# Performance work log

Measured on AMD Instinct MI355X. Metric: run time of the kernel, lower is better.

The kernel has to match this reference:

```python
import jax, jax.numpy as jnp
import numpy as np

SPIKING_T = 8        # args['spiking_t']
V_TH = 1.0           # spikingjelly IFNode default v_threshold
TAU = 2.0            # NonSpikingLIFNode tau
ALPHA = 4.0          # spikingjelly default Sigmoid surrogate alpha
MIN_LOG_STD, MAX_LOG_STD = -20.0, 2.0
LOG_2PI = float(np.log(2.0 * np.pi))

@jax.custom_vjp
def spike(x):
    # Heaviside forward (spikingjelly surrogate.Sigmoid behavior)
    return (x >= 0.0).astype(x.dtype)

def _spike_fwd(x):
    return spike(x), x

def _spike_bwd(x, g):
    s = jax.nn.sigmoid(ALPHA * x)
    return (g * ALPHA * s * (1.0 - s),)

spike.defvjp(_spike_fwd, _spike_bwd)


def setup_inputs() -> dict:
    key = jax.random.key(0)
    ks = jax.random.split(key, 8)
    B, N, H, A = 8192, 128, 1024, 32
    def lin_w(k, fan_in, fan_out):
        return jax.random.normal(k, (fan_in, fan_out), dtype=jnp.float32) / jnp.sqrt(float(fan_in))
    return {
        "state": jax.random.normal(ks[0], (B, N), dtype=jnp.float32),
        "w1": lin_w(ks[1], N, H),
        "b1": jnp.full((H,), 1e-6, dtype=jnp.float32),
        "w2": lin_w(ks[2], H, H),
        "b2": jnp.full((H,), 1e-6, dtype=jnp.float32),
        "w3": lin_w(ks[3], H, 2 * A),
        "b3": jnp.full((2 * A,), 1e-6, dtype=jnp.float32),
        "eps": jax.random.normal(ks[4], (B, A), dtype=jnp.float32),
    }


def reference(state, w1, b1, w2, b2, w3, b3, eps):
    B = state.shape[0]
    H = w1.shape[1]
    O = w3.shape[1]
    v1 = jnp.zeros((B, H), state.dtype)
    v2 = jnp.zeros((B, H), state.dtype)
    v3 = jnp.zeros((B, O), state.dtype)

    def step(carry, _):
        v1, v2, v3 = carry
        # IF node 1: charge, fire, hard reset to 0
        h1 = v1 + state @ w1 + b1
        s1 = spike(h1 - V_TH)
        v1 = h1 * (1.0 - s1)
        # IF node 2
        h2 = v2 + s1 @ w2 + b2
        s2 = spike(h2 - V_TH)
        v2 = h2 * (1.0 - s2)
        # NonSpiking LIF (decay_input=True, v_reset=0): v += (x - v)/tau
        x3 = s2 @ w3 + b3
        v3 = v3 + (x3 - v3) / TAU
        return (v1, v2, v3), None

    (v1, v2, v3), _ = jax.lax.scan(step, (v1, v2, v3), None, length=SPIKING_T)

    mu, log_std = jnp.split(v3, 2, axis=-1)
    log_std = jnp.clip(log_std, MIN_LOG_STD, MAX_LOG_STD)
    std = jnp.exp(log_std)
    z = mu + std * eps            # Normal rsample
    action = jnp.tanh(z)
    # Normal(mu, std).log_prob(z) = -eps^2/2 - log_std - 0.5*log(2*pi)
    log_prob = (-0.5 * eps * eps - log_std - 0.5 * LOG_2PI) \
               - jnp.log(1.0 - action * action + 1e-7)
    log_prob = jnp.sum(log_prob, axis=-1, keepdims=True)
    return action, log_prob
```

## Files before the change

### kernel.cpp

```cpp
#include <hip/hip_runtime.h>

typedef float    f32x4 __attribute__((ext_vector_type(4)));
typedef int      i32x4 __attribute__((ext_vector_type(4)));
typedef unsigned u32x4 __attribute__((ext_vector_type(4)));

typedef const __attribute__((address_space(1))) void* gptr_t;
typedef __attribute__((address_space(3))) void* lptr_t;

__device__ __forceinline__ void gload_lds16(const void* g, void* l) {
  __builtin_amdgcn_global_load_lds((gptr_t)g, (lptr_t)l, 16, 0, 0);
}

constexpr int Bsz  = 8192;
constexpr int Nin  = 128;
constexpr int Hd   = 1024;
constexpr int Aact = 32;
constexpr int Od   = 64;
constexpr int KC = 384;
constexpr float DELTA = 1.5e-4f;
constexpr unsigned WCAP = 262144;

__global__ void wsplit_i8_3_kernel(const float* __restrict__ src,
                                   char* __restrict__ p1, char* __restrict__ p2,
                                   char* __restrict__ p3, int N, int K) {
  const int lane = threadIdx.x;
  const int l15 = lane & 15, quad = lane >> 4;
  const int pn = blockIdx.x;
  const int kb = blockIdx.y;
  const int n = pn * 16 + l15;
  const int k0 = kb * 64 + quad * 16;
  char o1[16], o2[16], o3[16];
#pragma unroll
  for (int e = 0; e < 16; ++e) {
    float w = src[(size_t)(k0 + e) * N + n];
    float m1 = rintf(w * 512.0f);
    float r1 = w - m1 * (1.0f / 512.0f);
    float m2 = rintf(r1 * 65536.0f);
    float r2 = r1 - m2 * (1.0f / 65536.0f);
    float m3 = rintf(r2 * 8388608.0f);
    o1[e] = (char)(int)m1; o2[e] = (char)(int)m2; o3[e] = (char)(int)m3;
  }
  size_t off = ((size_t)pn * (K / 64) + kb) * 1024 + (size_t)lane * 16;
#pragma unroll
  for (int e = 0; e < 16; ++e) {
    p1[off + e] = o1[e]; p2[off + e] = o2[e]; p3[off + e] = o3[e];
  }
}

__global__ void wsplit_i8_kernel(const float* __restrict__ src,
                                 char* __restrict__ p1, char* __restrict__ p2,
                                 char* __restrict__ p3, char* __restrict__ p4,
                                 int N, int K) {
  const int lane = threadIdx.x;
  const int l15 = lane & 15, quad = lane >> 4;
  const int pn = blockIdx.x;
  const int kb = blockIdx.y;
  const int n = pn * 16 + l15;
  const int k0 = kb * 64 + quad * 16;
  char o1[16], o2[16], o3[16], o4[16];
#pragma unroll
  for (int e = 0; e < 16; ++e) {
    float w = src[(size_t)(k0 + e) * N + n];
    float m1 = rintf(w * 512.0f);
    float r1 = w - m1 * (1.0f / 512.0f);
    float m2 = rintf(r1 * 65536.0f);
    float r2 = r1 - m2 * (1.0f / 65536.0f);
    float m3 = rintf(r2 * 8388608.0f);
    float r3 = r2 - m3 * (1.0f / 8388608.0f);
    float m4 = rintf(r3 * 1073741824.0f);
    o1[e] = (char)(int)m1; o2[e] = (char)(int)m2;
    o3[e] = (char)(int)m3; o4[e] = (char)(int)m4;
  }
  size_t off = ((size_t)pn * (K / 64) + kb) * 1024 + (size_t)lane * 16;
#pragma unroll
  for (int e = 0; e < 16; ++e) {
    p1[off + e] = o1[e]; p2[off + e] = o2[e];
    p3[off + e] = o3[e]; p4[off + e] = o4[e];
  }
}

__global__ void transpose_f32_kernel(const float* __restrict__ src,
                                     float* __restrict__ dst, int R, int C) {
  __shared__ float tile[32][33];
  int c0 = blockIdx.x * 32, r0 = blockIdx.y * 32;
  for (int i = threadIdx.y; i < 32; i += 8)
    tile[i][threadIdx.x] = src[(size_t)(r0 + i) * C + c0 + threadIdx.x];
  __syncthreads();
  for (int i = threadIdx.y; i < 32; i += 8)
    dst[(size_t)(c0 + i) * R + r0 + threadIdx.x] = tile[threadIdx.x][i];
}

__global__ __launch_bounds__(256)
void x1_kernel(const float* __restrict__ state, const float* __restrict__ w1,
               const float* __restrict__ b1, unsigned char* __restrict__ s1pack) {
  __shared__ float sA[64][129];
  __shared__ float sB[128][68];
  const int m0 = blockIdx.x * 64, n0 = blockIdx.y * 64;
  const int tid = threadIdx.x;
  for (int idx = tid; idx < 64 * 32; idx += 256) {
    int r = idx >> 5, c4 = (idx & 31) << 2;
    float4 v = *(const float4*)(state + (size_t)(m0 + r) * Nin + c4);
    sA[r][c4] = v.x; sA[r][c4 + 1] = v.y; sA[r][c4 + 2] = v.z; sA[r][c4 + 3] = v.w;
  }
  for (int idx = tid; idx < 128 * 16; idx += 256) {
    int r = idx >> 4, c4 = (idx & 15) << 2;
    *(float4*)&sB[r][c4] = *(const float4*)(w1 + (size_t)r * Hd + n0 + c4);
  }
  __syncthreads();
  const int tx = tid & 15, ty = tid >> 4;
  float acc[4][4] = {};
  for (int k = 0; k < 128; ++k) {
    float a[4];
#pragma unroll
    for (int i = 0; i < 4; ++i) a[i] = sA[ty * 4 + i][k];
    float4 b = *(const float4*)&sB[k][tx * 4];
#pragma unroll
    for (int i = 0; i < 4; ++i) {
      acc[i][0] = __fmaf_rn(a[i], b.x, acc[i][0]);
      acc[i][1] = __fmaf_rn(a[i], b.y, acc[i][1]);
      acc[i][2] = __fmaf_rn(a[i], b.z, acc[i][2]);
      acc[i][3] = __fmaf_rn(a[i], b.w, acc[i][3]);
    }
  }
#pragma unroll
  for (int i = 0; i < 4; ++i) {
    int m = m0 + ty * 4 + i;
    unsigned pack = 0;
#pragma unroll
    for (int j = 0; j < 4; ++j) {
      int n = n0 + tx * 4 + j;
      float x = acc[i][j];
      float bb = b1[n];
      float v = 0.0f;
      unsigned bits = 0;
#pragma unroll
      for (int t = 0; t < 8; ++t) {
        float h = __fadd_rn(__fadd_rn(v, x), bb);
        if (h >= 1.0f) { bits |= (1u << t); v = 0.0f; } else { v = h; }
      }
      pack |= bits << (8 * j);
    }
    *(unsigned*)(s1pack + (size_t)m * Hd + n0 + tx * 4) = pack;
  }
}

__global__ __launch_bounds__(256, 3)
void gemm2i8_kernel(const unsigned char* __restrict__ s1pack,
                    const char* __restrict__ q1, const char* __restrict__ q2,
                    const char* __restrict__ q3,
                    const float* __restrict__ b2,
                    unsigned char* __restrict__ s2p,
                    unsigned* __restrict__ wcnt, unsigned* __restrict__ wlist) {
  constexpr int NKB = Hd / 64;
  __shared__ __align__(16) unsigned char lA[3][64 * 64];
  __shared__ __align__(16) char lB[3][3072];
  const int tid = threadIdx.x;
  const int m0 = blockIdx.x * 64;
  const int n0 = blockIdx.y * 16;
  const int wave = tid >> 6, lane = tid & 63, l15 = lane & 15, quad = lane >> 4;
  const char* bplane = (wave == 0) ? q1 : (wave == 1) ? q2 : q3;
  const unsigned char* asrc = s1pack
      + (size_t)(m0 + ((tid >> 6) << 4) + (tid & 15)) * Hd + ((tid >> 4) & 3) * 16;
  const char* bsrc2 = bplane + (size_t)blockIdx.y * NKB * 1024 + (size_t)lane * 16;
  i32x4 acc[3][8] = {};

  auto stage = [&](int kb, int buf) {
    gload_lds16(asrc + kb * 64, &lA[buf][tid * 16]);
    if (wave < 3)
      gload_lds16(bsrc2 + (size_t)kb * 1024, &lB[buf][wave * 1024 + lane * 16]);
  };
  stage(0, 0); stage(1, 1);

#pragma unroll
  for (int kb = 0; kb < NKB; ++kb) {
    const int cur = kb % 3;
    if (kb < NKB - 1) {
      if (wave < 3) asm volatile("s_waitcnt vmcnt(2)" ::: "memory");
      else          asm volatile("s_waitcnt vmcnt(1)" ::: "memory");
    } else {
      asm volatile("s_waitcnt vmcnt(0)" ::: "memory");
    }
    __builtin_amdgcn_s_barrier();
    asm volatile("" ::: "memory");
    u32x4 ad = *(const u32x4*)&lA[cur][wave * 1024 + lane * 16];
    i32x4 fb0 = *(const i32x4*)&lB[cur][lane * 16];
    i32x4 fb1 = *(const i32x4*)&lB[cur][1024 + lane * 16];
    i32x4 fb2 = *(const i32x4*)&lB[cur][2048 + lane * 16];
    if (kb + 2 < NKB) stage(kb + 2, (kb + 2) % 3);
    __builtin_amdgcn_s_setprio(1);
#pragma unroll
    for (int t = 0; t < 8; ++t) {
      i32x4 af;
      af[0] = (int)((ad[0] >> t) & 0x01010101u);
      af[1] = (int)((ad[1] >> t) & 0x01010101u);
      af[2] = (int)((ad[2] >> t) & 0x01010101u);
      af[3] = (int)((ad[3] >> t) & 0x01010101u);
      acc[0][t] = __builtin_amdgcn_mfma_i32_16x16x64_i8(af, fb0, acc[0][t], 0, 0, 0);
      acc[1][t] = __builtin_amdgcn_mfma_i32_16x16x64_i8(af, fb1, acc[1][t], 0, 0, 0);
      acc[2][t] = __builtin_amdgcn_mfma_i32_16x16x64_i8(af, fb2, acc[2][t], 0, 0, 0);
    }
    __builtin_amdgcn_s_setprio(0);
  }
  const int n = n0 + l15;
  const float bb = b2[n];
#pragma unroll
  for (int r = 0; r < 4; ++r) {
    int m = m0 + wave * 16 + quad * 4 + r;
    size_t idx = (size_t)m * Hd + n;
    float v = 0.0f;
    unsigned bits = 0;
#pragma unroll
    for (int t = 0; t < 8; ++t) {
      double ge = (double)acc[0][t][r] * 1.953125e-3
                + (double)acc[1][t][r] * 1.52587890625e-5
                + (double)acc[2][t][r] * 1.1920928955078125e-7;
      float G = (float)ge;
      float h = __fadd_rn(__fadd_rn(v, G), bb);
      if (__builtin_expect(__builtin_fabsf(h - 1.0f) < DELTA, 0)) {
        unsigned pos = atomicAdd(wcnt, 1u);
        if (pos < WCAP) wlist[pos] = (unsigned)idx;
      }
      bool sp = (h >= 1.0f);
      if (sp) bits |= (1u << t);
      v = sp ? 0.0f : h;
    }
    s2p[idx] = (unsigned char)bits;
  }
}

__global__ __launch_bounds__(256)
void fixup_kernel(const unsigned* __restrict__ wcnt, const unsigned* __restrict__ wlist,
                  const unsigned char* __restrict__ s1pack, const float* __restrict__ w2tf,
                  const float* __restrict__ b2, unsigned char* __restrict__ s2p) {
  unsigned cnt = *wcnt;
  if (cnt > WCAP) cnt = WCAP;
  const int tid = threadIdx.x;
  const int lane = tid & 63;
  const int sl = lane / 3, blk3 = lane - sl * 3;
  const int wid = blockIdx.x * (blockDim.x >> 6) + (tid >> 6);
  const int nwaves = gridDim.x * (blockDim.x >> 6);
  for (unsigned base = (unsigned)wid * 21u; base < cnt; base += (unsigned)nwaves * 21u) {
    unsigned site = base + (unsigned)sl;
    bool act = (sl < 21) && (site < cnt);
    unsigned idx = act ? wlist[site] : 0u;
    int m = (int)(idx >> 10), n = (int)(idx & 1023u);
    const unsigned char* prow = s1pack + ((size_t)m << 10);
    const float* col = w2tf + ((size_t)n << 10);
    int kb = blk3 * KC;
    int kend = (blk3 == 2) ? Hd : kb + KC;
    float S[8] = {};
    if (act) {
      for (int k = kb; k < kend; k += 8) {
        float4 wa = *(const float4*)(col + k);
        float4 wb = *(const float4*)(col + k + 4);
        unsigned b0 = *(const unsigned*)(prow + k);
        unsigned b1 = *(const unsigned*)(prow + k + 4);
#pragma unroll
        for (int tau = 0; tau < 8; ++tau) {
          S[tau] = __fadd_rn(S[tau], ((b0 >> tau) & 1)        ? wa.x : 0.0f);
          S[tau] = __fadd_rn(S[tau], ((b0 >> (8 + tau)) & 1)  ? wa.y : 0.0f);
          S[tau] = __fadd_rn(S[tau], ((b0 >> (16 + tau)) & 1) ? wa.z : 0.0f);
          S[tau] = __fadd_rn(S[tau], ((b0 >> (24 + tau)) & 1) ? wa.w : 0.0f);
          S[tau] = __fadd_rn(S[tau], ((b1 >> tau) & 1)        ? wb.x : 0.0f);
          S[tau] = __fadd_rn(S[tau], ((b1 >> (8 + tau)) & 1)  ? wb.y : 0.0f);
          S[tau] = __fadd_rn(S[tau], ((b1 >> (16 + tau)) & 1) ? wb.z : 0.0f);
          S[tau] = __fadd_rn(S[tau], ((b1 >> (24 + tau)) & 1) ? wb.w : 0.0f);
        }
      }
    }
    float G[8];
#pragma unroll
    for (int tau = 0; tau < 8; ++tau) {
      float sB = __shfl(S[tau], lane + 1);
      float sC = __shfl(S[tau], lane + 2);
      G[tau] = __fadd_rn(__fadd_rn(S[tau], sB), sC);
    }
    if (act && blk3 == 0) {
      float bb = b2[n];
      float v = 0.0f;
      unsigned bits = 0;
      for (int tau = 0; tau < 8; ++tau) {
        float h = __fadd_rn(__fadd_rn(v, G[tau]), bb);
        bool sp = (h >= 1.0f);
        if (sp) bits |= (1u << tau);
        v = sp ? 0.0f : h;
      }
      s2p[idx] = (unsigned char)bits;
    }
  }
}

__global__ __launch_bounds__(256, 2)
void gemm3i8_kernel(const unsigned char* __restrict__ s2p,
                    const char* __restrict__ q1, const char* __restrict__ q2,
                    const char* __restrict__ q3, const char* __restrict__ q4,
                    const float* __restrict__ b3, float* __restrict__ v3) {
  constexpr int NKB = Hd / 64;
  __shared__ __align__(16) unsigned char lA[3][64 * 64];
  __shared__ __align__(16) char lB[3][4096];
  const int tid = threadIdx.x;
  const int m0 = blockIdx.x * 64;
  const int n0 = blockIdx.y * 16;
  const int wave = tid >> 6, lane = tid & 63, l15 = lane & 15, quad = lane >> 4;
  const char* bsrc = (wave == 0) ? q1 : (wave == 1) ? q2 : (wave == 2) ? q3 : q4;
  const unsigned char* asrc = s2p
      + (size_t)(m0 + ((tid >> 6) << 4) + (tid & 15)) * Hd + ((tid >> 4) & 3) * 16;
  const char* bsrc2 = bsrc + (size_t)blockIdx.y * NKB * 1024 + (size_t)lane * 16;
  i32x4 acc[4][8] = {};
  u32x4 fa[2]; i32x4 fb[2][4];

  auto stage = [&](int kb, int buf) {
    gload_lds16(asrc + kb * 64, &lA[buf][tid * 16]);
    gload_lds16(bsrc2 + (size_t)kb * 1024, &lB[buf][tid * 16]);
  };
  stage(0, 0); stage(1, 1);
  __syncthreads();
  fa[0] = *(const u32x4*)&lA[0][wave * 1024 + lane * 16];
#pragma unroll
  for (int p = 0; p < 4; ++p)
    fb[0][p] = *(const i32x4*)&lB[0][p * 1024 + lane * 16];

#pragma unroll
  for (int kb = 0; kb < NKB; ++kb) {
    const int cur = kb & 1, nxt = cur ^ 1;
    if (kb + 1 < NKB) {
      asm volatile("s_waitcnt vmcnt(0)" ::: "memory");
      __builtin_amdgcn_s_barrier();
      asm volatile("" ::: "memory");
      const int rb = (kb + 1) % 3;
      fa[nxt] = *(const u32x4*)&lA[rb][wave * 1024 + lane * 16];
#pragma unroll
      for (int p = 0; p < 4; ++p)
        fb[nxt][p] = *(const i32x4*)&lB[rb][p * 1024 + lane * 16];
      if (kb + 2 < NKB) stage(kb + 2, (kb + 2) % 3);
    }
#pragma unroll
    for (int t = 0; t < 8; ++t) {
      i32x4 af;
      af[0] = (int)((fa[cur][0] >> t) & 0x01010101u);
      af[1] = (int)((fa[cur][1] >> t) & 0x01010101u);
      af[2] = (int)((fa[cur][2] >> t) & 0x01010101u);
      af[3] = (int)((fa[cur][3] >> t) & 0x01010101u);
#pragma unroll
      for (int p = 0; p < 4; ++p)
        acc[p][t] = __builtin_amdgcn_mfma_i32_16x16x64_i8(af, fb[cur][p], acc[p][t], 0, 0, 0);
    }
  }
  const int n = n0 + l15;
  const float bb = b3[n];
#pragma unroll
  for (int r = 0; r < 4; ++r) {
    int m = m0 + wave * 16 + quad * 4 + r;
    float v = 0.0f;
#pragma unroll
    for (int t = 0; t < 8; ++t) {
      double ge = (double)acc[0][t][r] * 1.953125e-3
                + (double)acc[1][t][r] * 1.52587890625e-5
                + (double)acc[2][t][r] * 1.1920928955078125e-7
                + (double)acc[3][t][r] * 9.31322574615478515625e-10;
      float x3 = __fadd_rn((float)ge, bb);
      float dd = __fsub_rn(x3, v);
      v = __fadd_rn(v, __fmul_rn(dd, 0.5f));
    }
    v3[(size_t)m * Od + n] = v;
  }
}

__global__ void final_kernel(const float* __restrict__ v3, const float* __restrict__ eps,
                             float* __restrict__ action, float* __restrict__ logp) {
  int tid = threadIdx.x;
  int row = blockIdx.x * 8 + (tid >> 5);
  int j = tid & 31;
  float mu = v3[(size_t)row * Od + j];
  float ls = v3[(size_t)row * Od + 32 + j];
  ls = fminf(fmaxf(ls, -20.0f), 2.0f);
  float sd = (float)exp((double)ls);
  float e  = eps[(size_t)row * Aact + j];
  float z  = __fadd_rn(mu, __fmul_rn(sd, e));
  float a;
  if (__builtin_fabsf(z) >= 7.90531111f) a = __builtin_copysignf(1.0f, z);
  else                                   a = (float)tanh((double)z);
  float aa = __fmul_rn(a, a);
  float u  = __fadd_rn(__fsub_rn(1.0f, aa), 1e-7f);
  float lg = (float)log((double)u);
  float l  = __fmul_rn(__fmul_rn(-0.5f, e), e);
  l = __fsub_rn(l, ls);
  l = __fsub_rn(l, 0.9189385332046727f);
  float term = __fsub_rn(l, lg);
  action[(size_t)row * Aact + j] = a;
  double lp = (double)term;
#pragma unroll
  for (int w = 16; w >= 1; w >>= 1) lp += __shfl_xor(lp, w);
  if (j == 0) logp[row] = (float)lp;
}

extern "C" void kernel_launch(void* const* d_in, const int* in_sizes, int n_in,
                              void* d_out, int out_size, void* d_ws, size_t ws_size,
                              hipStream_t stream) {
  const float* state = (const float*)d_in[0];
  const float* w1 = (const float*)d_in[1];
  const float* b1 = (const float*)d_in[2];
  const float* w2 = (const float*)d_in[3];
  const float* b2 = (const float*)d_in[4];
  const float* w3 = (const float*)d_in[5];
  const float* b3 = (const float*)d_in[6];
  const float* eps = (const float*)d_in[7];
  float* out_action = (float*)d_out;
  float* out_logp = out_action + (size_t)Bsz * Aact;

  char* p = (char*)d_ws;
  auto take = [&](size_t bytes) {
    char* r = p;
    p += (bytes + 255) & ~(size_t)255;
    return r;
  };
  float* v3f = (float*)take((size_t)Bsz * Od * 4);
  unsigned char* s1pack = (unsigned char*)take((size_t)Bsz * Hd);
  unsigned char* s2p = (unsigned char*)take((size_t)Bsz * Hd);
  char* w2q1 = (char*)take((size_t)Hd * Hd);
  char* w2q2 = (char*)take((size_t)Hd * Hd);
  char* w2q3 = (char*)take((size_t)Hd * Hd);
  char* w3q1 = (char*)take((size_t)Hd * Od);
  char* w3q2 = (char*)take((size_t)Hd * Od);
  char* w3q3 = (char*)take((size_t)Hd * Od);
  char* w3q4 = (char*)take((size_t)Hd * Od);
  float* w2tf = (float*)take((size_t)Hd * Hd * 4);
  unsigned* wcnt = (unsigned*)take(8 * 4);
  unsigned* wlist = (unsigned*)take((size_t)WCAP * 4);

  wsplit_i8_3_kernel<<<dim3(Hd / 16, Hd / 64), 64, 0, stream>>>(w2, w2q1, w2q2, w2q3, Hd, Hd);
  wsplit_i8_kernel<<<dim3(Od / 16, Hd / 64), 64, 0, stream>>>(w3, w3q1, w3q2, w3q3, w3q4, Od, Hd);
  transpose_f32_kernel<<<dim3(Hd / 32, Hd / 32), dim3(32, 8), 0, stream>>>(w2, w2tf, Hd, Hd);
  x1_kernel<<<dim3(Bsz / 64, Hd / 64), 256, 0, stream>>>(state, w1, b1, s1pack);
  hipMemsetAsync(wcnt, 0, 8 * 4, stream);

  gemm2i8_kernel<<<dim3(Bsz / 64, Hd / 16), 256, 0, stream>>>(s1pack, w2q1, w2q2, w2q3,
                                                              b2, s2p, wcnt, wlist);
  fixup_kernel<<<128, 256, 0, stream>>>(wcnt, wlist, s1pack, w2tf, b2, s2p);

  gemm3i8_kernel<<<dim3(Bsz / 64, Od / 16), 256, 0, stream>>>(s2p, w3q1, w3q2, w3q3, w3q4,
                                                              b3, v3f);
  final_kernel<<<Bsz / 8, 256, 0, stream>>>(v3f, eps, out_action, out_logp);
}
```

Measured before the change: 326.7 us.

## Fuse weight-prep kernels, stage two K-blocks per barrier, drop fourth W3 plane

Merges the W2 and W3 int8 plane splits and the W2 transpose into one launch. The transpose is written directly per thread, so stores are uncoalesced. Both int8 GEMMs now load two K-blocks per barrier using a six-deep LDS ring, which halves the barrier count at the cost of more shared memory. The third-layer GEMM drops its fourth weight plane, cutting MFMA work and loads, and gains a higher occupancy hint. This loses low-order precision in W3, which could change results near thresholds.

```diff
diff --git a/kernel.cpp b/kernel.cpp
--- a/kernel.cpp
+++ b/kernel.cpp
@@ -20,74 +20,48 @@
 constexpr float DELTA = 1.5e-4f;
 constexpr unsigned WCAP = 262144;
 
-__global__ void wsplit_i8_3_kernel(const float* __restrict__ src,
-                                   char* __restrict__ p1, char* __restrict__ p2,
-                                   char* __restrict__ p3, int N, int K) {
+__global__ void wsplit_all_kernel(const float* __restrict__ w2, const float* __restrict__ w3,
+                                  char* __restrict__ p1, char* __restrict__ p2,
+                                  char* __restrict__ p3,
+                                  char* __restrict__ r1, char* __restrict__ r2,
+                                  char* __restrict__ r3,
+                                  float* __restrict__ w2tf) {
   const int lane = threadIdx.x;
   const int l15 = lane & 15, quad = lane >> 4;
   const int pn = blockIdx.x;
   const int kb = blockIdx.y;
-  const int n = pn * 16 + l15;
+  const bool isw3 = (pn >= Hd / 16);
+  const int pnl = isw3 ? pn - Hd / 16 : pn;
+  const float* src = isw3 ? w3 : w2;
+  const int N = isw3 ? Od : Hd;
+  const int n = pnl * 16 + l15;
   const int k0 = kb * 64 + quad * 16;
+  char* d1 = isw3 ? r1 : p1;
+  char* d2 = isw3 ? r2 : p2;
+  char* d3 = isw3 ? r3 : p3;
+  float wv[16];
   char o1[16], o2[16], o3[16];
 #pragma unroll
   for (int e = 0; e < 16; ++e) {
     float w = src[(size_t)(k0 + e) * N + n];
+    wv[e] = w;
     float m1 = rintf(w * 512.0f);
-    float r1 = w - m1 * (1.0f / 512.0f);
-    float m2 = rintf(r1 * 65536.0f);
-    float r2 = r1 - m2 * (1.0f / 65536.0f);
-    float m3 = rintf(r2 * 8388608.0f);
+    float q1 = w - m1 * (1.0f / 512.0f);
+    float m2 = rintf(q1 * 65536.0f);
+    float q2 = q1 - m2 * (1.0f / 65536.0f);
+    float m3 = rintf(q2 * 8388608.0f);
     o1[e] = (char)(int)m1; o2[e] = (char)(int)m2; o3[e] = (char)(int)m3;
   }
-  size_t off = ((size_t)pn * (K / 64) + kb) * 1024 + (size_t)lane * 16;
+  size_t off = ((size_t)pnl * 16 + kb) * 1024 + (size_t)lane * 16;
 #pragma unroll
   for (int e = 0; e < 16; ++e) {
-    p1[off + e] = o1[e]; p2[off + e] = o2[e]; p3[off + e] = o3[e];
-  }
-}
-
-__global__ void wsplit_i8_kernel(const float* __restrict__ src,
-                                 char* __restrict__ p1, char* __restrict__ p2,
-                                 char* __restrict__ p3, char* __restrict__ p4,
-                                 int N, int K) {
-  const int lane = threadIdx.x;
-  const int l15 = lane & 15, quad = lane >> 4;
-  const int pn = blockIdx.x;
-  const int kb = blockIdx.y;
-  const int n = pn * 16 + l15;
-  const int k0 = kb * 64 + quad * 16;
-  char o1[16], o2[16], o3[16], o4[16];
-#pragma unroll
-  for (int e = 0; e < 16; ++e) {
-    float w = src[(size_t)(k0 + e) * N + n];
-    float m1 = rintf(w * 512.0f);
-    float r1 = w - m1 * (1.0f / 512.0f);
-    float m2 = rintf(r1 * 65536.0f);
-    float r2 = r1 - m2 * (1.0f / 65536.0f);
-    float m3 = rintf(r2 * 8388608.0f);
-    float r3 = r2 - m3 * (1.0f / 8388608.0f);
-    float m4 = rintf(r3 * 1073741824.0f);
-    o1[e] = (char)(int)m1; o2[e] = (char)(int)m2;
-    o3[e] = (char)(int)m3; o4[e] = (char)(int)m4;
-  }
-  size_t off = ((size_t)pn * (K / 64) + kb) * 1024 + (size_t)lane * 16;
-#pragma unroll
-  for (int e = 0; e < 16; ++e) {
-    p1[off + e] = o1[e]; p2[off + e] = o2[e];
-    p3[off + e] = o3[e]; p4[off + e] = o4[e];
-  }
-}
-
-__global__ void transpose_f32_kernel(const float* __restrict__ src,
-                                     float* __restrict__ dst, int R, int C) {
-  __shared__ float tile[32][33];
-  int c0 = blockIdx.x * 32, r0 = blockIdx.y * 32;
-  for (int i = threadIdx.y; i < 32; i += 8)
-    tile[i][threadIdx.x] = src[(size_t)(r0 + i) * C + c0 + threadIdx.x];
-  __syncthreads();
-  for (int i = threadIdx.y; i < 32; i += 8)
-    dst[(size_t)(c0 + i) * R + r0 + threadIdx.x] = tile[threadIdx.x][i];
+    d1[off + e] = o1[e]; d2[off + e] = o2[e]; d3[off + e] = o3[e];
+  }
+  if (!isw3) {
+#pragma unroll
+    for (int e = 0; e < 16; ++e)
+      w2tf[(size_t)n * Hd + k0 + e] = wv[e];
+  }
 }
 
 __global__ __launch_bounds__(256)
@@ -152,8 +126,9 @@
                     unsigned char* __restrict__ s2p,
                     unsigned* __restrict__ wcnt, unsigned* __restrict__ wlist) {
   constexpr int NKB = Hd / 64;
-  __shared__ __align__(16) unsigned char lA[3][64 * 64];
-  __shared__ __align__(16) char lB[3][3072];
+  constexpr int NPH = NKB / 2;
+  __shared__ __align__(16) unsigned char lA[6][64 * 64];
+  __shared__ __align__(16) char lB[6][3072];
   const int tid = threadIdx.x;
   const int m0 = blockIdx.x * 64;
   const int n0 = blockIdx.y * 16;
@@ -164,42 +139,63 @@
   const char* bsrc2 = bplane + (size_t)blockIdx.y * NKB * 1024 + (size_t)lane * 16;
   i32x4 acc[3][8] = {};
 
-  auto stage = [&](int kb, int buf) {
-    gload_lds16(asrc + kb * 64, &lA[buf][tid * 16]);
+  auto stage2 = [&](int ph) {
+    int t0 = 2 * ph, t1 = t0 + 1;
+    gload_lds16(asrc + t0 * 64, &lA[t0 % 6][tid * 16]);
     if (wave < 3)
-      gload_lds16(bsrc2 + (size_t)kb * 1024, &lB[buf][wave * 1024 + lane * 16]);
+      gload_lds16(bsrc2 + (size_t)t0 * 1024, &lB[t0 % 6][wave * 1024 + lane * 16]);
+    gload_lds16(asrc + t1 * 64, &lA[t1 % 6][tid * 16]);
+    if (wave < 3)
+      gload_lds16(bsrc2 + (size_t)t1 * 1024, &lB[t1 % 6][wave * 1024 + lane * 16]);
   };
-  stage(0, 0); stage(1, 1);
-
-#pragma unroll
-  for (int kb = 0; kb < NKB; ++kb) {
-    const int cur = kb % 3;
-    if (kb < NKB - 1) {
-      if (wave < 3) asm volatile("s_waitcnt vmcnt(2)" ::: "memory");
-      else          asm volatile("s_waitcnt vmcnt(1)" ::: "memory");
+  stage2(0); stage2(1);
+
+#pragma unroll
+  for (int ph = 0; ph < NPH; ++ph) {
+    if (ph < NPH - 1) {
+      if (wave < 3) asm volatile("s_waitcnt vmcnt(4)" ::: "memory");
+      else          asm volatile("s_waitcnt vmcnt(2)" ::: "memory");
     } else {
       asm volatile("s_waitcnt vmcnt(0)" ::: "memory");
     }
     __builtin_amdgcn_s_barrier();
     asm volatile("" ::: "memory");
-    u32x4 ad = *(const u32x4*)&lA[cur][wave * 1024 + lane * 16];
-    i32x4 fb0 = *(const i32x4*)&lB[cur][lane * 16];
-    i32x4 fb1 = *(const i32x4*)&lB[cur][1024 + lane * 16];
-    i32x4 fb2 = *(const i32x4*)&lB[cur][2048 + lane * 16];
-    if (kb + 2 < NKB) stage(kb + 2, (kb + 2) % 3);
-    __builtin_amdgcn_s_setprio(1);
-#pragma unroll
-    for (int t = 0; t < 8; ++t) {
-      i32x4 af;
-      af[0] = (int)((ad[0] >> t) & 0x01010101u);
-      af[1] = (int)((ad[1] >> t) & 0x01010101u);
-      af[2] = (int)((ad[2] >> t) & 0x01010101u);
-      af[3] = (int)((ad[3] >> t) & 0x01010101u);
-      acc[0][t] = __builtin_amdgcn_mfma_i32_16x16x64_i8(af, fb0, acc[0][t], 0, 0, 0);
-      acc[1][t] = __builtin_amdgcn_mfma_i32_16x16x64_i8(af, fb1, acc[1][t], 0, 0, 0);
-      acc[2][t] = __builtin_amdgcn_mfma_i32_16x16x64_i8(af, fb2, acc[2][t], 0, 0, 0);
-    }
-    __builtin_amdgcn_s_setprio(0);
+    const int t0 = 2 * ph, t1 = t0 + 1;
+    {
+      u32x4 ad = *(const u32x4*)&lA[t0 % 6][wave * 1024 + lane * 16];
+      i32x4 fb0 = *(const i32x4*)&lB[t0 % 6][lane * 16];
+      i32x4 fb1 = *(const i32x4*)&lB[t0 % 6][1024 + lane * 16];
+      i32x4 fb2 = *(const i32x4*)&lB[t0 % 6][2048 + lane * 16];
+      if (ph + 2 < NPH) stage2(ph + 2);
+#pragma unroll
+      for (int t = 0; t < 8; ++t) {
+        i32x4 af;
+        af[0] = (int)((ad[0] >> t) & 0x01010101u);
+        af[1] = (int)((ad[1] >> t) & 0x01010101u);
+        af[2] = (int)((ad[2] >> t) & 0x01010101u);
+        af[3] = (int)((ad[3] >> t) & 0x01010101u);
+        acc[0][t] = __builtin_amdgcn_mfma_i32_16x16x64_i8(af, fb0, acc[0][t], 0, 0, 0);
+        acc[1][t] = __builtin_amdgcn_mfma_i32_16x16x64_i8(af, fb1, acc[1][t], 0, 0, 0);
+        acc[2][t] = __builtin_amdgcn_mfma_i32_16x16x64_i8(af, fb2, acc[2][t], 0, 0, 0);
+      }
+    }
+    {
+      u32x4 ad = *(const u32x4*)&lA[t1 % 6][wave * 1024 + lane * 16];
+      i32x4 fb0 = *(const i32x4*)&lB[t1 % 6][lane * 16];
+      i32x4 fb1 = *(const i32x4*)&lB[t1 % 6][1024 + lane * 16];
+      i32x4 fb2 = *(const i32x4*)&lB[t1 % 6][2048 + lane * 16];
+#pragma unroll
+      for (int t = 0; t < 8; ++t) {
+        i32x4 af;
+        af[0] = (int)((ad[0] >> t) & 0x01010101u);
+        af[1] = (int)((ad[1] >> t) & 0x01010101u);
+        af[2] = (int)((ad[2] >> t) & 0x01010101u);
+        af[3] = (int)((ad[3] >> t) & 0x01010101u);
+        acc[0][t] = __builtin_amdgcn_mfma_i32_16x16x64_i8(af, fb0, acc[0][t], 0, 0, 0);
+        acc[1][t] = __builtin_amdgcn_mfma_i32_16x16x64_i8(af, fb1, acc[1][t], 0, 0, 0);
+        acc[2][t] = __builtin_amdgcn_mfma_i32_16x16x64_i8(af, fb2, acc[2][t], 0, 0, 0);
+      }
+    }
   }
   const int n = n0 + l15;
   const float bb = b2[n];
@@ -290,60 +286,81 @@
   }
 }
 
-__global__ __launch_bounds__(256, 2)
+__global__ __launch_bounds__(256, 3)
 void gemm3i8_kernel(const unsigned char* __restrict__ s2p,
                     const char* __restrict__ q1, const char* __restrict__ q2,
-                    const char* __restrict__ q3, const char* __restrict__ q4,
+                    const char* __restrict__ q3,
                     const float* __restrict__ b3, float* __restrict__ v3) {
   constexpr int NKB = Hd / 64;
-  __shared__ __align__(16) unsigned char lA[3][64 * 64];
-  __shared__ __align__(16) char lB[3][4096];
+  constexpr int NPH = NKB / 2;
+  __shared__ __align__(16) unsigned char lA[6][64 * 64];
+  __shared__ __align__(16) char lB[6][3072];
   const int tid = threadIdx.x;
   const int m0 = blockIdx.x * 64;
   const int n0 = blockIdx.y * 16;
   const int wave = tid >> 6, lane = tid & 63, l15 = lane & 15, quad = lane >> 4;
-  const char* bsrc = (wave == 0) ? q1 : (wave == 1) ? q2 : (wave == 2) ? q3 : q4;
+  const char* bplane = (wave == 0) ? q1 : (wave == 1) ? q2 : q3;
   const unsigned char* asrc = s2p
       + (size_t)(m0 + ((tid >> 6) << 4) + (tid & 15)) * Hd + ((tid >> 4) & 3) * 16;
-  const char* bsrc2 = bsrc + (size_t)blockIdx.y * NKB * 1024 + (size_t)lane * 16;
-  i32x4 acc[4][8] = {};
-  u32x4 fa[2]; i32x4 fb[2][4];
-
-  auto stage = [&](int kb, int buf) {
-    gload_lds16(asrc + kb * 64, &lA[buf][tid * 16]);
-    gload_lds16(bsrc2 + (size_t)kb * 1024, &lB[buf][tid * 16]);
+  const char* bsrc2 = bplane + (size_t)blockIdx.y * NKB * 1024 + (size_t)lane * 16;
+  i32x4 acc[3][8] = {};
+
+  auto stage2 = [&](int ph) {
+    int t0 = 2 * ph, t1 = t0 + 1;
+    gload_lds16(asrc + t0 * 64, &lA[t0 % 6][tid * 16]);
+    if (wave < 3)
+      gload_lds16(bsrc2 + (size_t)t0 * 1024, &lB[t0 % 6][wave * 1024 + lane * 16]);
+    gload_lds16(asrc + t1 * 64, &lA[t1 % 6][tid * 16]);
+    if (wave < 3)
+      gload_lds16(bsrc2 + (size_t)t1 * 1024, &lB[t1 % 6][wave * 1024 + lane * 16]);
   };
-  stage(0, 0); stage(1, 1);
-  __syncthreads();
-  fa[0] = *(const u32x4*)&lA[0][wave * 1024 + lane * 16];
-#pragma unroll
-  for (int p = 0; p < 4; ++p)
-    fb[0][p] = *(const i32x4*)&lB[0][p * 1024 + lane * 16];
-
-#pragma unroll
-  for (int kb = 0; kb < NKB; ++kb) {
-    const int cur = kb & 1, nxt = cur ^ 1;
-    if (kb + 1 < NKB) {
+  stage2(0); stage2(1);
+
+#pragma unroll
+  for (int ph = 0; ph < NPH; ++ph) {
+    if (ph < NPH - 1) {
+      if (wave < 3) asm volatile("s_waitcnt vmcnt(4)" ::: "memory");
+      else          asm volatile("s_waitcnt vmcnt(2)" ::: "memory");
+    } else {
       asm volatile("s_waitcnt vmcnt(0)" ::: "memory");
-      __builtin_amdgcn_s_barrier();
-      asm volatile("" ::: "memory");
-      const int rb = (kb + 1) % 3;
-      fa[nxt] = *(const u32x4*)&lA[rb][wave * 1024 + lane * 16];
-#pragma unroll
-      for (int p = 0; p < 4; ++p)
-        fb[nxt][p] = *(const i32x4*)&lB[rb][p * 1024 + lane * 16];
-      if (kb + 2 < NKB) stage(kb + 2, (kb + 2) % 3);
-    }
-#pragma unroll
-    for (int t = 0; t < 8; ++t) {
-      i32x4 af;
-      af[0] = (int)((fa[cur][0] >> t) & 0x01010101u);
-      af[1] = (int)((fa[cur][1] >> t) & 0x01010101u);
-      af[2] = (int)((fa[cur][2] >> t) & 0x01010101u);
-      af[3] = (int)((fa[cur][3] >> t) & 0x01010101u);
-#pragma unroll
-      for (int p = 0; p < 4; ++p)
-        acc[p][t] = __builtin_amdgcn_mfma_i32_16x16x64_i8(af, fb[cur][p], acc[p][t], 0, 0, 0);
+    }
+    __builtin_amdgcn_s_barrier();
+    asm volatile("" ::: "memory");
+    const int t0 = 2 * ph, t1 = t0 + 1;
+    {
+      u32x4 ad = *(const u32x4*)&lA[t0 % 6][wave * 1024 + lane * 16];
+      i32x4 fb0 = *(const i32x4*)&lB[t0 % 6][lane * 16];
+      i32x4 fb1 = *(const i32x4*)&lB[t0 % 6][1024 + lane * 16];
+      i32x4 fb2 = *(const i32x4*)&lB[t0 % 6][2048 + lane * 16];
+      if (ph + 2 < NPH) stage2(ph + 2);
+#pragma unroll
+      for (int t = 0; t < 8; ++t) {
+        i32x4 af;
+        af[0] = (int)((ad[0] >> t) & 0x01010101u);
+        af[1] = (int)((ad[1] >> t) & 0x01010101u);
+        af[2] = (int)((ad[2] >> t) & 0x01010101u);
+        af[3] = (int)((ad[3] >> t) & 0x01010101u);
+        acc[0][t] = __builtin_amdgcn_mfma_i32_16x16x64_i8(af, fb0, acc[0][t], 0, 0, 0);
+        acc[1][t] = __builtin_amdgcn_mfma_i32_16x16x64_i8(af, fb1, acc[1][t], 0, 0, 0);
+        acc[2][t] = __builtin_amdgcn_mfma_i32_16x16x64_i8(af, fb2, acc[2][t], 0, 0, 0);
+      }
+    }
+    {
+      u32x4 ad = *(const u32x4*)&lA[t1 % 6][wave * 1024 + lane * 16];
+      i32x4 fb0 = *(const i32x4*)&lB[t1 % 6][lane * 16];
+      i32x4 fb1 = *(const i32x4*)&lB[t1 % 6][1024 + lane * 16];
+      i32x4 fb2 = *(const i32x4*)&lB[t1 % 6][2048 + lane * 16];
+#pragma unroll
+      for (int t = 0; t < 8; ++t) {
+        i32x4 af;
+        af[0] = (int)((ad[0] >> t) & 0x01010101u);
+        af[1] = (int)((ad[1] >> t) & 0x01010101u);
+        af[2] = (int)((ad[2] >> t) & 0x01010101u);
+        af[3] = (int)((ad[3] >> t) & 0x01010101u);
+        acc[0][t] = __builtin_amdgcn_mfma_i32_16x16x64_i8(af, fb0, acc[0][t], 0, 0, 0);
+        acc[1][t] = __builtin_amdgcn_mfma_i32_16x16x64_i8(af, fb1, acc[1][t], 0, 0, 0);
+        acc[2][t] = __builtin_amdgcn_mfma_i32_16x16x64_i8(af, fb2, acc[2][t], 0, 0, 0);
+      }
     }
   }
   const int n = n0 + l15;
@@ -356,8 +373,7 @@
     for (int t = 0; t < 8; ++t) {
       double ge = (double)acc[0][t][r] * 1.953125e-3
                 + (double)acc[1][t][r] * 1.52587890625e-5
-                + (double)acc[2][t][r] * 1.1920928955078125e-7
-                + (double)acc[3][t][r] * 9.31322574615478515625e-10;
+                + (double)acc[2][t][r] * 1.1920928955078125e-7;
       float x3 = __fadd_rn((float)ge, bb);
       float dd = __fsub_rn(x3, v);
       v = __fadd_rn(v, __fmul_rn(dd, 0.5f));
@@ -423,14 +439,12 @@
   char* w3q1 = (char*)take((size_t)Hd * Od);
   char* w3q2 = (char*)take((size_t)Hd * Od);
   char* w3q3 = (char*)take((size_t)Hd * Od);
-  char* w3q4 = (char*)take((size_t)Hd * Od);
   float* w2tf = (float*)take((size_t)Hd * Hd * 4);
   unsigned* wcnt = (unsigned*)take(8 * 4);
   unsigned* wlist = (unsigned*)take((size_t)WCAP * 4);
 
-  wsplit_i8_3_kernel<<<dim3(Hd / 16, Hd / 64), 64, 0, stream>>>(w2, w2q1, w2q2, w2q3, Hd, Hd);
-  wsplit_i8_kernel<<<dim3(Od / 16, Hd / 64), 64, 0, stream>>>(w3, w3q1, w3q2, w3q3, w3q4, Od, Hd);
-  transpose_f32_kernel<<<dim3(Hd / 32, Hd / 32), dim3(32, 8), 0, stream>>>(w2, w2tf, Hd, Hd);
+  wsplit_all_kernel<<<dim3(Hd / 16 + Od / 16, Hd / 64), 64, 0, stream>>>(
+      w2, w3, w2q1, w2q2, w2q3, w3q1, w3q2, w3q3, w2tf);
   x1_kernel<<<dim3(Bsz / 64, Hd / 64), 256, 0, stream>>>(state, w1, b1, s1pack);
   hipMemsetAsync(wcnt, 0, 8 * 4, stream);
 
@@ -438,7 +452,7 @@
                                                               b2, s2p, wcnt, wlist);
   fixup_kernel<<<128, 256, 0, stream>>>(wcnt, wlist, s1pack, w2tf, b2, s2p);
 
-  gemm3i8_kernel<<<dim3(Bsz / 64, Od / 16), 256, 0, stream>>>(s2p, w3q1, w3q2, w3q3, w3q4,
+  gemm3i8_kernel<<<dim3(Bsz / 64, Od / 16), 256, 0, stream>>>(s2p, w3q1, w3q2, w3q3,
                                                               b3, v3f);
   final_kernel<<<Bsz / 8, 256, 0, stream>>>(v3f, eps, out_action, out_logp);
 }
```

Result: faster. 320.2 us (-2.0%).
